# Kernel tuning notes

Hardware: AMD Instinct MI355X
Metric: run time of the kernel (lower is better)

## Reference

```python
import jax, jax.numpy as jnp
import numpy as np

N, T, D_IN, D_OUT = 131072, 16, 128, 128


def setup_inputs() -> dict:
    key = jax.random.key(0)
    k1, k2, k3, k4 = jax.random.split(key, 4)
    x = jax.random.normal(k1, (N, D_IN), dtype=jnp.float32)
    # sorted type ids, matching HeteroLinear(is_sorted=True)
    type_vec = jnp.sort(jax.random.randint(k2, (N,), 0, T)).astype(jnp.int32)
    # HeteroLinear weight: [num_types, in_channels, out_channels]; out = x @ W[t] + b[t]
    weight = (jax.random.normal(k3, (T, D_IN, D_OUT), dtype=jnp.float32)
              / np.float32(np.sqrt(D_IN)))
    bias = jax.random.normal(k4, (T, D_OUT), dtype=jnp.float32) * 0.01
    return {"x": x, "type_vec": type_vec, "weight": weight, "bias": bias}


def _grouped_matmul(x, weight, type_vec):
    """Segment (grouped) matmul: rows are sorted by type; row i uses weight[type_vec[i]]."""
    try:
        # Native grouped-GEMM primitive (exploits is_sorted=True contiguity).
        group_sizes = jnp.bincount(type_vec, length=weight.shape[0]).astype(jnp.int32)
        return jax.lax.ragged_dot(x, weight, group_sizes)
    except Exception:
        # Fallback: small fixed loop over the T types, masked accumulate.
        out = jnp.zeros((x.shape[0], weight.shape[-1]), dtype=x.dtype)
        for t in range(weight.shape[0]):
            out = out + jnp.where((type_vec == t)[:, None], x @ weight[t], jnp.zeros((), x.dtype))
        return out


def reference(x, type_vec, weight, bias):
    # ToHeteroLinear.fused_forward == HeteroLinear(x, type_vec):
    #   out[i] = x[i] @ weight[type_vec[i]] + bias[type_vec[i]]
    out = _grouped_matmul(x, weight, type_vec)  # [N, D_OUT]
    return out + bias[type_vec]
```

## Files before the change

### kernel.cpp

```cpp
#include <hip/hip_runtime.h>

#define DD 128
#define BM 64
#define CHUNK 4
#define T_TYPES 16

typedef __bf16 bf16x8 __attribute__((ext_vector_type(8)));
typedef __bf16 bf16x4 __attribute__((ext_vector_type(4)));
typedef float  f32x4  __attribute__((ext_vector_type(4)));

__device__ __forceinline__ void async_copy16(const void* g, void* l) {
    __builtin_amdgcn_global_load_lds(
        (const __attribute__((address_space(1))) unsigned int*)g,
        (__attribute__((address_space(3))) unsigned int*)l, 16, 0, 0);
}

__global__ __launch_bounds__(256) void transpose_w_frag_kernel(
    const float* __restrict__ w, unsigned short* __restrict__ wbf)
{
    __shared__ float lds[DD * 33];
    const int t   = blockIdx.x >> 2;
    const int n0  = (blockIdx.x & 3) * 32;
    const int tid = threadIdx.x;
    const float* wt = w + (size_t)t * DD * DD;

    #pragma unroll
    for (int i = 0; i < 4; ++i) {
        int f = tid + i * 256;
        int k = f >> 3;
        int c = (f & 7) * 4;
        float4 v = *(const float4*)&wt[k * DD + n0 + c];
        lds[k * 33 + c + 0] = v.x;
        lds[k * 33 + c + 1] = v.y;
        lds[k * 33 + c + 2] = v.z;
        lds[k * 33 + c + 3] = v.w;
    }
    __syncthreads();
    #pragma unroll
    for (int i = 0; i < 4; ++i) {
        int g  = tid + i * 256;
        int nl = g >> 5;
        int k4 = (g & 31) * 4;
        int n  = n0 + nl;
        int nt  = n >> 4, n16 = n & 15;
        int kk  = k4 >> 5, q = (k4 >> 3) & 3, jb = k4 & 7;
        int lane = q * 16 + n16;
        size_t ofs = ((((size_t)t * 8 + nt) * 4 + kk) * 64 + lane) * 8 + jb;
        ushort4 o;
        union { __bf16 b; unsigned short u; } cv;
        cv.b = (__bf16)lds[(k4 + 0) * 33 + nl]; o.x = cv.u;
        cv.b = (__bf16)lds[(k4 + 1) * 33 + nl]; o.y = cv.u;
        cv.b = (__bf16)lds[(k4 + 2) * 33 + nl]; o.z = cv.u;
        cv.b = (__bf16)lds[(k4 + 3) * 33 + nl]; o.w = cv.u;
        *(ushort4*)&wbf[ofs] = o;
    }
}

__global__ __launch_bounds__(256, 2) void hetero_main_kernel(
    const float* __restrict__ x,
    const int*   __restrict__ tv,
    const __bf16* __restrict__ wbf,
    const float* __restrict__ bias,
    float*       __restrict__ out)
{
    __shared__ __bf16 As[4 * 16 * DD];
    __shared__ __bf16 Bs[DD * DD];

    const int tid  = threadIdx.x;
    const int wave = tid >> 6;
    const int lane = tid & 63;
    const int q    = lane >> 4;
    const int n16  = lane & 15;
    const int chunk0 = blockIdx.x * (BM * CHUNK);

    __bf16* Aq = &As[wave * 16 * DD];

    int t_res = tv[chunk0];

    {
        const char* gsrc = (const char*)(wbf + (size_t)t_res * DD * DD);
        char* ldst = (char*)Bs;
        const int wofs = wave * 1024 + lane * 16;
        #pragma unroll
        for (int r = 0; r < 8; ++r)
            async_copy16(gsrc + r * 4096 + wofs, ldst + r * 4096 + wave * 1024);
    }

    float bv[8];
    #pragma unroll
    for (int nt = 0; nt < 8; ++nt) bv[nt] = bias[t_res * DD + nt * 16 + n16];

    float4 xf[8];
    {
        const float4* p = (const float4*)(x + (size_t)(chunk0 + wave * 16) * DD);
        #pragma unroll
        for (int j = 0; j < 8; ++j) xf[j] = p[lane + 64 * j];
    }

    __syncthreads();

    #pragma unroll
    for (int tile = 0; tile < CHUNK; ++tile) {
        const int trow0 = chunk0 + tile * BM;
        const int wrow0 = trow0 + wave * 16;

        float4 xn[8];
        if (tile + 1 < CHUNK) {
            const float4* p = (const float4*)(x + (size_t)(wrow0 + BM) * DD);
            #pragma unroll
            for (int j = 0; j < 8; ++j) xn[j] = p[lane + 64 * j];
        }

        #pragma unroll
        for (int j = 0; j < 8; ++j) {
            int f  = lane + 64 * j;
            int r  = f >> 5;
            int c4 = (f & 31) << 2;
            int g  = c4 >> 3;
            bf16x4 pk;
            pk[0] = (__bf16)xf[j].x; pk[1] = (__bf16)xf[j].y;
            pk[2] = (__bf16)xf[j].z; pk[3] = (__bf16)xf[j].w;
            *(bf16x4*)&Aq[r * DD + (((g ^ (r & 7)) << 3) | (c4 & 7))] = pk;
        }

        bf16x8 a[4];
        #pragma unroll
        for (int kk = 0; kk < 4; ++kk) {
            int gr = ((kk << 2) | q) ^ (n16 & 7);
            a[kk] = *(const bf16x8*)&Aq[n16 * DD + (gr << 3)];
        }

        const int tlo = tv[trow0];
        const int thi = tv[trow0 + BM - 1];

        for (int t = tlo; t <= thi; ++t) {
            if (t != t_res) {
                __syncthreads();
                const char* gsrc = (const char*)(wbf + (size_t)t * DD * DD);
                char* ldst = (char*)Bs;
                const int wofs = wave * 1024 + lane * 16;
                #pragma unroll
                for (int r = 0; r < 8; ++r)
                    async_copy16(gsrc + r * 4096 + wofs, ldst + r * 4096 + wave * 1024);
                t_res = t;
                #pragma unroll
                for (int nt = 0; nt < 8; ++nt) bv[nt] = bias[t * DD + nt * 16 + n16];
                __syncthreads();
            }

            f32x4 acc[8];
            #pragma unroll
            for (int nt = 0; nt < 8; ++nt) acc[nt] = (f32x4){0.f, 0.f, 0.f, 0.f};

            #pragma unroll
            for (int nt = 0; nt < 8; ++nt) {
                #pragma unroll
                for (int kk = 0; kk < 4; ++kk) {
                    bf16x8 b = *(const bf16x8*)&Bs[(((nt << 2) | kk) << 9) | (lane << 3)];
                    acc[nt] = __builtin_amdgcn_mfma_f32_16x16x32_bf16(a[kk], b, acc[nt], 0, 0, 0);
                }
            }

            const int rbase = wrow0 + q * 4;
            bool m0 = true, m1 = true, m2 = true, m3 = true;
            if (tlo != thi) {
                m0 = (tv[rbase + 0] == t);
                m1 = (tv[rbase + 1] == t);
                m2 = (tv[rbase + 2] == t);
                m3 = (tv[rbase + 3] == t);
            }
            float* o = out + (size_t)rbase * DD + n16;
            #pragma unroll
            for (int nt = 0; nt < 8; ++nt) {
                float* oc = o + nt * 16;
                if (m0) oc[0 * DD] = acc[nt][0] + bv[nt];
                if (m1) oc[1 * DD] = acc[nt][1] + bv[nt];
                if (m2) oc[2 * DD] = acc[nt][2] + bv[nt];
                if (m3) oc[3 * DD] = acc[nt][3] + bv[nt];
            }
        }

        #pragma unroll
        for (int j = 0; j < 8; ++j) xf[j] = xn[j];
    }
}

extern "C" void kernel_launch(void* const* d_in, const int* in_sizes, int n_in,
                              void* d_out, int out_size, void* d_ws, size_t ws_size,
                              hipStream_t stream) {
    const float* x    = (const float*)d_in[0];
    const int*   tv   = (const int*)d_in[1];
    const float* w    = (const float*)d_in[2];
    const float* bias = (const float*)d_in[3];
    float*       out  = (float*)d_out;
    unsigned short* wbf = (unsigned short*)d_ws;

    int nrows = in_sizes[0] / DD;
    int grid  = nrows / (BM * CHUNK);

    hipLaunchKernelGGL(transpose_w_frag_kernel, dim3(T_TYPES * 4), dim3(256), 0, stream,
                       w, wbf);
    hipLaunchKernelGGL(hetero_main_kernel, dim3(grid), dim3(256), 0, stream,
                       x, tv, (const __bf16*)wbf, bias, out);
}
```

Measured before the change: 121.3 us.

## Load x directly into MFMA fragment layout, drop A LDS staging, raise occupancy

Each lane now loads the x values it needs for the MFMA A operand straight from global memory and converts them to bf16 in registers, so the swizzled LDS staging buffer for A and its round trip go away. With less LDS per block, the launch bounds ask for three blocks per CU, and CHUNK is halved so the grid has twice as many blocks. The global loads become 32-byte strided per lane instead of fully coalesced float4 rows, and the smaller chunks mean the per-type weight tile is reloaded into LDS more often across blocks.

```diff
diff --git a/kernel.cpp b/kernel.cpp
--- a/kernel.cpp
+++ b/kernel.cpp
@@ -2,11 +2,10 @@
 
 #define DD 128
 #define BM 64
-#define CHUNK 4
+#define CHUNK 2
 #define T_TYPES 16
 
 typedef __bf16 bf16x8 __attribute__((ext_vector_type(8)));
-typedef __bf16 bf16x4 __attribute__((ext_vector_type(4)));
 typedef float  f32x4  __attribute__((ext_vector_type(4)));
 
 __device__ __forceinline__ void async_copy16(const void* g, void* l) {
@@ -56,14 +55,13 @@
     }
 }
 
-__global__ __launch_bounds__(256, 2) void hetero_main_kernel(
+__global__ __launch_bounds__(256, 3) void hetero_main_kernel(
     const float* __restrict__ x,
     const int*   __restrict__ tv,
     const __bf16* __restrict__ wbf,
     const float* __restrict__ bias,
     float*       __restrict__ out)
 {
-    __shared__ __bf16 As[4 * 16 * DD];
     __shared__ __bf16 Bs[DD * DD];
 
     const int tid  = threadIdx.x;
@@ -72,8 +70,6 @@
     const int q    = lane >> 4;
     const int n16  = lane & 15;
     const int chunk0 = blockIdx.x * (BM * CHUNK);
-
-    __bf16* Aq = &As[wave * 16 * DD];
 
     int t_res = tv[chunk0];
 
@@ -90,11 +86,14 @@
     #pragma unroll
     for (int nt = 0; nt < 8; ++nt) bv[nt] = bias[t_res * DD + nt * 16 + n16];
 
-    float4 xf[8];
+    f32x4 xlo[4], xhi[4];
     {
-        const float4* p = (const float4*)(x + (size_t)(chunk0 + wave * 16) * DD);
+        const float* base = x + (size_t)(chunk0 + wave * 16 + n16) * DD + q * 8;
         #pragma unroll
-        for (int j = 0; j < 8; ++j) xf[j] = p[lane + 64 * j];
+        for (int kk = 0; kk < 4; ++kk) {
+            xlo[kk] = *(const f32x4*)(base + kk * 32);
+            xhi[kk] = *(const f32x4*)(base + kk * 32 + 4);
+        }
     }
 
     __syncthreads();
@@ -104,30 +103,25 @@
         const int trow0 = chunk0 + tile * BM;
         const int wrow0 = trow0 + wave * 16;
 
-        float4 xn[8];
+        f32x4 nlo[4], nhi[4];
         if (tile + 1 < CHUNK) {
-            const float4* p = (const float4*)(x + (size_t)(wrow0 + BM) * DD);
+            const float* base = x + (size_t)(wrow0 + BM + n16) * DD + q * 8;
             #pragma unroll
-            for (int j = 0; j < 8; ++j) xn[j] = p[lane + 64 * j];
-        }
-
-        #pragma unroll
-        for (int j = 0; j < 8; ++j) {
-            int f  = lane + 64 * j;
-            int r  = f >> 5;
-            int c4 = (f & 31) << 2;
-            int g  = c4 >> 3;
-            bf16x4 pk;
-            pk[0] = (__bf16)xf[j].x; pk[1] = (__bf16)xf[j].y;
-            pk[2] = (__bf16)xf[j].z; pk[3] = (__bf16)xf[j].w;
-            *(bf16x4*)&Aq[r * DD + (((g ^ (r & 7)) << 3) | (c4 & 7))] = pk;
+            for (int kk = 0; kk < 4; ++kk) {
+                nlo[kk] = *(const f32x4*)(base + kk * 32);
+                nhi[kk] = *(const f32x4*)(base + kk * 32 + 4);
+            }
         }
 
         bf16x8 a[4];
         #pragma unroll
         for (int kk = 0; kk < 4; ++kk) {
-            int gr = ((kk << 2) | q) ^ (n16 & 7);
-            a[kk] = *(const bf16x8*)&Aq[n16 * DD + (gr << 3)];
+            bf16x8 t;
+            t[0] = (__bf16)xlo[kk][0]; t[1] = (__bf16)xlo[kk][1];
+            t[2] = (__bf16)xlo[kk][2]; t[3] = (__bf16)xlo[kk][3];
+            t[4] = (__bf16)xhi[kk][0]; t[5] = (__bf16)xhi[kk][1];
+            t[6] = (__bf16)xhi[kk][2]; t[7] = (__bf16)xhi[kk][3];
+            a[kk] = t;
         }
 
         const int tlo = tv[trow0];
@@ -181,7 +175,7 @@
         }
 
         #pragma unroll
-        for (int j = 0; j < 8; ++j) xf[j] = xn[j];
+        for (int kk = 0; kk < 4; ++kk) { xlo[kk] = nlo[kk]; xhi[kk] = nhi[kk]; }
     }
 }
 
```

New measurement: 123.8 us. 2.1% more time.
